# Kernel tuning notes

Measured on AMD Instinct MI355X. Metric: run time of the kernel, lower is better.

## Reference

```python
import jax, jax.numpy as jnp
import numpy as np

N_NODES = 50000
N_EDGES = 1_600_000
IN_FEAT = 64
HIDDEN = 64
OUT_FEAT = 10
NUM_LAYERS = 8
ALPHA = 0.1
THETA = 0.5
LN_EPS = 1e-5


def setup_inputs() -> dict:
    key = jax.random.key(0)
    ks = jax.random.split(key, 6)
    N, E, Fin, H, C = N_NODES, N_EDGES, IN_FEAT, HIDDEN, OUT_FEAT
    return {
        "x": jax.random.normal(ks[0], (N, Fin), jnp.float32),
        "W_lin": jax.random.normal(ks[1], (Fin, H), jnp.float32) / np.float32(np.sqrt(Fin)),
        "b_lin": jnp.zeros((H,), jnp.float32),
        "Ws": jax.random.normal(ks[2], (NUM_LAYERS, H, H), jnp.float32) / np.float32(np.sqrt(H)),
        "W1": jax.random.normal(ks[3], (2 * H, H), jnp.float32) / np.float32(np.sqrt(2 * H)),
        "b1": jnp.zeros((H,), jnp.float32),
        "ln_g": jnp.ones((H,), jnp.float32),
        "ln_b": jnp.zeros((H,), jnp.float32),
        "W2": jax.random.normal(ks[4], (H, C), jnp.float32) / np.float32(np.sqrt(H)),
        "b2": jnp.zeros((C,), jnp.float32),
        "edge_index": jax.random.randint(ks[5], (2, E), 0, N, jnp.int32),
    }


def _gcn_norm(edge_index, n):
    # PyG gcn_norm: add self-loops, symmetric D^-1/2 A D^-1/2 normalization.
    loop = jnp.arange(n, dtype=edge_index.dtype)
    row = jnp.concatenate([edge_index[0], loop])
    col = jnp.concatenate([edge_index[1], loop])
    w = jnp.ones(row.shape[0], jnp.float32)
    deg = jax.ops.segment_sum(w, col, num_segments=n)
    dinv = jnp.where(deg > 0, jax.lax.rsqrt(deg), 0.0)
    return row, col, dinv[row] * dinv[col]


def reference(x, W_lin, b_lin, Ws, W1, b1, ln_g, ln_b, W2, b2, edge_index):
    n = x.shape[0]
    row, col, vals = _gcn_norm(edge_index, n)
    h = jax.nn.relu(x @ W_lin + b_lin)  # [N, H]
    h0 = h
    for layer in range(NUM_LAYERS):
        beta = np.float32(np.log(THETA / (layer + 1) + 1.0))
        # SpMM: out[i] = sum over edges (i<-j) vals * h[j]
        agg = jax.ops.segment_sum(vals[:, None] * h[col], row, num_segments=n)
        mix = (1.0 - ALPHA) * agg + ALPHA * h0  # GCN2 initial-residual
        h = jax.nn.relu((1.0 - beta) * mix + beta * (mix @ Ws[layer]))  # identity mapping
    # mix_node_features 'cat': gather endpoint features per edge -> [E, 2H]
    line_x = jnp.concatenate([h[edge_index[0]], h[edge_index[1]]], axis=-1)
    # ClassifierMLP2: Linear -> LayerNorm -> ReLU -> Linear
    z = line_x @ W1 + b1
    mu = jnp.mean(z, axis=-1, keepdims=True)
    var = jnp.var(z, axis=-1, keepdims=True)
    z = (z - mu) * jax.lax.rsqrt(var + LN_EPS) * ln_g + ln_b
    z = jax.nn.relu(z)
    return z @ W2 + b2  # [E, out_features]
```

## Files before the change

### kernel.cpp

```cpp
#include <hip/hip_runtime.h>
#include <hip/hip_fp16.h>
#include <math.h>

#define N_NODES 50000
#define N_EDGES 1600000
#define EDGE_GRID 2048
#define CAP 128

#define NB 64
#define BRANGE 782
#define BCAP 28672
#define BIN_BLOCKS 512
#define EPB (N_EDGES/BIN_BLOCKS)
#define CURPAD 32

using half8  = __attribute__((ext_vector_type(8))) _Float16;
using half4  = __attribute__((ext_vector_type(4))) _Float16;
using float4v = __attribute__((ext_vector_type(4))) float;

__device__ __forceinline__ float rl(float v, int srclane){
  return __int_as_float(__builtin_amdgcn_readlane(__float_as_int(v), srclane));
}

__global__ __launch_bounds__(256) void k_bin(const int* __restrict__ rowE, const int* __restrict__ colE,
                                             unsigned* __restrict__ rstream, unsigned short* __restrict__ cstream,
                                             int* __restrict__ rcur, int* __restrict__ ccur){
  __shared__ int hr[NB], hc[NB], br[NB], bc[NB];
  int t = threadIdx.x;
  if(t < NB){ hr[t] = 0; hc[t] = 0; }
  __syncthreads();
  int e0 = blockIdx.x * EPB;
  for(int e = e0 + t; e < e0 + EPB; e += 256){
    int r = __builtin_nontemporal_load(rowE + e);
    int c = __builtin_nontemporal_load(colE + e);
    atomicAdd(&hr[r/BRANGE], 1);
    atomicAdd(&hc[c/BRANGE], 1);
  }
  __syncthreads();
  if(t < NB){
    br[t] = atomicAdd(&rcur[t*CURPAD], hr[t]); hr[t] = 0;
    bc[t] = atomicAdd(&ccur[t*CURPAD], hc[t]); hc[t] = 0;
  }
  __syncthreads();
  for(int e = e0 + t; e < e0 + EPB; e += 256){
    int r = rowE[e];
    int c = colE[e];
    int rb = r/BRANGE, cb = c/BRANGE;
    int rp = br[rb] + atomicAdd(&hr[rb], 1);
    int cp = bc[cb] + atomicAdd(&hc[cb], 1);
    if(rp < BCAP) rstream[(size_t)rb*BCAP + rp] = ((unsigned)r << 16) | (unsigned)c;
    if(cp < BCAP) cstream[(size_t)cb*BCAP + cp] = (unsigned short)c;
  }
}

__global__ __launch_bounds__(256) void k_build(const unsigned* __restrict__ rstream,
                                               const unsigned short* __restrict__ cstream,
                                               const int* __restrict__ rcur, const int* __restrict__ ccur,
                                               int* __restrict__ row_fill, int* __restrict__ degcnt,
                                               unsigned short* __restrict__ csr_col){
  __shared__ int lf[BRANGE];
  int b = blockIdx.x & (NB-1);
  int role = blockIdx.x >> 6;
  int base = b*BRANGE;
  int range = min(BRANGE, N_NODES - base);
  int t = threadIdx.x;
  for(int i=t;i<range;i+=256) lf[i] = 0;
  __syncthreads();
  if(role == 0){
    int cnt = min(rcur[b*CURPAD], BCAP);
    const unsigned* sp = rstream + (size_t)b*BCAP;
    for(int i=t;i<cnt;i+=256){
      unsigned rc = sp[i];
      int r = (int)(rc >> 16), c = (int)(rc & 0xffffu);
      int pos = atomicAdd(&lf[r-base], 1);
      if(pos < CAP) csr_col[(size_t)r*CAP + pos] = (unsigned short)c;
    }
    __syncthreads();
    for(int i=t;i<range;i+=256) row_fill[base+i] = lf[i];
  } else {
    int cnt = min(ccur[b*CURPAD], BCAP);
    const unsigned short* sp = cstream + (size_t)b*BCAP;
    for(int i=t;i<cnt;i+=256){
      int c = (int)sp[i];
      atomicAdd(&lf[c-base], 1);
    }
    __syncthreads();
    for(int i=t;i<range;i+=256) degcnt[base+i] = lf[i];
  }
}

__global__ void k_dinv(int* __restrict__ degcnt_rdeg, float* __restrict__ dinv,
                       __half* __restrict__ gA, __half* __restrict__ gB){
  int i = blockIdx.x*256 + threadIdx.x;
  if(i < N_NODES){
    float dp1 = (float)(degcnt_rdeg[i] + 1);
    dinv[i] = rsqrtf(dp1);
    ((float*)degcnt_rdeg)[i] = sqrtf(dp1);
  }
  if(i < 64){
    gA[(size_t)N_NODES*64 + i] = __float2half(0.f);
    gB[(size_t)N_NODES*64 + i] = __float2half(0.f);
  }
}


__global__ __launch_bounds__(256) void k_lin0(const float* __restrict__ x, const float* __restrict__ W,
                                              const float* __restrict__ b, const float* __restrict__ dinv,
                                              __half* __restrict__ h0, __half* __restrict__ g0){
  __shared__ float Wl[4096];
  int t = threadIdx.x;
  for(int i=t;i<4096;i+=256) Wl[i] = W[i];
  __syncthreads();
  int wave = t>>6, lane = t&63;
  int row0 = blockIdx.x*16 + wave*4;
  float4 xq = ((const float4*)(x + (size_t)row0*64))[lane];
  float a0=0,a1=0,a2=0,a3=0;
  #pragma unroll
  for(int k=0;k<64;k++){
    float w = Wl[k*64+lane];
    float comp = ((k&3)==0)?xq.x:((k&3)==1)?xq.y:((k&3)==2)?xq.z:xq.w;
    a0 += rl(comp,      (k>>2)) * w;
    a1 += rl(comp, 16 + (k>>2)) * w;
    a2 += rl(comp, 32 + (k>>2)) * w;
    a3 += rl(comp, 48 + (k>>2)) * w;
  }
  float bb = b[lane];
  float h[4] = {fmaxf(a0+bb,0.f), fmaxf(a1+bb,0.f), fmaxf(a2+bb,0.f), fmaxf(a3+bb,0.f)};
  #pragma unroll
  for(int r=0;r<4;r++){
    float dv = dinv[row0+r];
    h0[(size_t)(row0+r)*64+lane] = __float2half(h[r]);
    g0[(size_t)(row0+r)*64+lane] = __float2half(dv*h[r]);
  }
}

__global__ __launch_bounds__(256) void k_ab(const __half* __restrict__ g, const float* __restrict__ rdeg,
                                            const float* __restrict__ W1,
                                            __half* __restrict__ A, __half* __restrict__ B){
  __shared__ float Wa[4096];
  __shared__ float Wb[4096];
  int t = threadIdx.x;
  for(int i=t;i<4096;i+=256){ Wa[i] = W1[i]; Wb[i] = W1[4096+i]; }
  __syncthreads();
  int wave = t>>6, lane = t&63;
  int row0 = blockIdx.x*16 + wave*4;
  int myrow = row0 + (lane>>4);
  float rd = rdeg[myrow];
  const __half2* hp = (const __half2*)(g + (size_t)row0*64);
  __half2 p01 = hp[2*lane], p23 = hp[2*lane+1];
  float2 f01 = __half22float2(p01), f23 = __half22float2(p23);
  float4 xq = make_float4(f01.x*rd, f01.y*rd, f23.x*rd, f23.y*rd);
  float a0=0,a1=0,a2=0,a3=0,b0=0,b1=0,b2=0,b3=0;
  #pragma unroll
  for(int k=0;k<64;k++){
    float wa = Wa[k*64+lane], wb = Wb[k*64+lane];
    float comp = ((k&3)==0)?xq.x:((k&3)==1)?xq.y:((k&3)==2)?xq.z:xq.w;
    float s0 = rl(comp,      (k>>2));
    float s1 = rl(comp, 16 + (k>>2));
    float s2 = rl(comp, 32 + (k>>2));
    float s3 = rl(comp, 48 + (k>>2));
    a0 += s0*wa; a1 += s1*wa; a2 += s2*wa; a3 += s3*wa;
    b0 += s0*wb; b1 += s1*wb; b2 += s2*wb; b3 += s3*wb;
  }
  A[(size_t)(row0+0)*64+lane]=__float2half(a0); A[(size_t)(row0+1)*64+lane]=__float2half(a1);
  A[(size_t)(row0+2)*64+lane]=__float2half(a2); A[(size_t)(row0+3)*64+lane]=__float2half(a3);
  B[(size_t)(row0+0)*64+lane]=__float2half(b0); B[(size_t)(row0+1)*64+lane]=__float2half(b1);
  B[(size_t)(row0+2)*64+lane]=__float2half(b2); B[(size_t)(row0+3)*64+lane]=__float2half(b3);
}

__global__ __launch_bounds__(256) void k_layer(const __half* __restrict__ g_in, const __half* __restrict__ h0,
                          const int* __restrict__ row_fill, const unsigned short* __restrict__ csr_col,
                          const float* __restrict__ dinv,
                          const float* __restrict__ Wsl, float beta, __half* __restrict__ g_out){
  __shared__ __align__(16) _Float16 tile[16*72];
  int t = threadIdx.x, wave = t>>6, lane = t&63;
  int quad = lane>>4, l15 = lane&15;
  int grp = lane>>3, l8 = lane&7;

  half8 bfrag0, bfrag1;
  int n = 16*wave + l15;
  #pragma unroll
  for(int j=0;j<8;j++){
    int k0 = quad*8 + j;
    int k1 = 32 + quad*8 + j;
    float v0 = beta*Wsl[k0*64+n] + ((k0==n)?(1.f-beta):0.f);
    float v1 = beta*Wsl[k1*64+n] + ((k1==n)?(1.f-beta):0.f);
    bfrag0[j] = (_Float16)v0;
    bfrag1[j] = (_Float16)v1;
  }

  int i0 = blockIdx.x*16;
  int iw = i0 + 4*wave;

  int deg[4], cv[4];
  half8 selfv[4], h0v[4];
  float dv[4];
  #pragma unroll
  for(int r=0;r<4;r++) deg[r] = min(row_fill[iw+r], CAP);
  #pragma unroll
  for(int r=0;r<4;r++){
    const unsigned short* colp = csr_col + (size_t)(iw+r)*CAP;
    cv[r] = (lane < deg[r]) ? (int)__builtin_nontemporal_load(colp + lane) : 0;
  }
  #pragma unroll
  for(int r=0;r<4;r++){
    dv[r]    = dinv[iw+r];
    selfv[r] = *(const half8*)(g_in + (size_t)(iw+r)*64 + 8*l8);
    h0v[r]   = *(const half8*)(h0   + (size_t)(iw+r)*64 + 8*l8);
  }

  for(int r=0;r<4;r++){
    const unsigned short* colp = csr_col + (size_t)(iw+r)*CAP;
    float acc[8] = {0,0,0,0,0,0,0,0};
    int base = 0;
    int cur  = cv[r];
    for(;;){
      int rem = deg[r] - base; if(rem > 64) rem = 64;
      int nit = (rem + 7) >> 3;
      int it = 0;
      for(; it+2<=nit; it+=2){
        int iA = 8*it + grp, iB = iA + 8;
        int cA = __shfl(cur, iA, 64); cA = (iA < rem) ? cA : N_NODES;
        int cB = __shfl(cur, iB, 64); cB = (iB < rem) ? cB : N_NODES;
        half8 vA = *(const half8*)(g_in + (size_t)cA*64 + 8*l8);
        half8 vB = *(const half8*)(g_in + (size_t)cB*64 + 8*l8);
        #pragma unroll
        for(int k=0;k<8;k++) acc[k] += (float)vA[k] + (float)vB[k];
      }
      if(it < nit){
        int iA = 8*it + grp;
        int cA = __shfl(cur, iA, 64); cA = (iA < rem) ? cA : N_NODES;
        half8 vA = *(const half8*)(g_in + (size_t)cA*64 + 8*l8);
        #pragma unroll
        for(int k=0;k<8;k++) acc[k] += (float)vA[k];
      }
      base += 64;
      if(base >= deg[r]) break;
      cur = (base + lane < deg[r]) ? (int)__builtin_nontemporal_load(colp + base + lane) : 0;
    }
    #pragma unroll
    for(int k=0;k<8;k++){
      acc[k] += __shfl_xor(acc[k], 8, 64);
      acc[k] += __shfl_xor(acc[k], 16, 64);
      acc[k] += __shfl_xor(acc[k], 32, 64);
    }
    if(grp == 0){
      half8 mixv;
      #pragma unroll
      for(int k=0;k<8;k++){
        float m = 0.9f*dv[r]*(acc[k] + (float)selfv[r][k]) + 0.1f*(float)h0v[r][k];
        mixv[k] = (_Float16)m;
      }
      *(half8*)&tile[(4*wave+r)*72 + 8*l8] = mixv;
    }
  }
  __syncthreads();

  float4v acc4 = {0.f,0.f,0.f,0.f};
  half8 afrag0 = *(const half8*)&tile[l15*72 + quad*8];
  half8 afrag1 = *(const half8*)&tile[l15*72 + quad*8 + 32];
  acc4 = __builtin_amdgcn_mfma_f32_16x16x32_f16(afrag0, bfrag0, acc4, 0,0,0);
  acc4 = __builtin_amdgcn_mfma_f32_16x16x32_f16(afrag1, bfrag1, acc4, 0,0,0);
  #pragma unroll
  for(int r=0;r<4;r++){
    int row = quad*4 + r;
    float dvo = dinv[i0+row];
    g_out[(size_t)(i0+row)*64 + n] = __float2half(dvo*fmaxf(acc4[r], 0.f));
  }
}

__global__ __launch_bounds__(256) void k_edge(const __half* __restrict__ A, const __half* __restrict__ B,
                         const int* __restrict__ srcE, const int* __restrict__ dstE,
                         const float* __restrict__ b1v, const float* __restrict__ lng,
                         const float* __restrict__ lnb, const float* __restrict__ W2,
                         const float* __restrict__ b2v, float* __restrict__ out){
  int t = threadIdx.x, wave = t>>6, lane = t&63;
  int l15 = lane&15, quad = lane>>4;

  half8 bf0, bf1;
  #pragma unroll
  for(int j=0;j<8;j++){
    float w0 = (l15<10) ? W2[(quad*8+j)*10 + l15]    : 0.f;
    float w1 = (l15<10) ? W2[(32+quad*8+j)*10 + l15] : 0.f;
    bf0[j] = (_Float16)w0;
    bf1[j] = (_Float16)w1;
  }
  float b1r0[8], b1r1[8], gr0[8], gr1[8], br0[8], br1[8];
  #pragma unroll
  for(int j=0;j<8;j++){
    b1r0[j] = b1v[quad*8+j];    b1r1[j] = b1v[32+quad*8+j];
    gr0[j]  = lng[quad*8+j];    gr1[j]  = lng[32+quad*8+j];
    br0[j]  = lnb[quad*8+j];    br1[j]  = lnb[32+quad*8+j];
  }
  float bias = (l15<10) ? b2v[l15] : 0.f;

  for(int eb = blockIdx.x*64 + wave*16; eb < N_EDGES; eb += EDGE_GRID*64){
    int e = eb + l15;
    int s = __builtin_nontemporal_load(srcE + e);
    int d = __builtin_nontemporal_load(dstE + e);
    half8 a0 = *(const half8*)(A + (size_t)s*64 + quad*8);
    half8 a1 = *(const half8*)(A + (size_t)s*64 + 32 + quad*8);
    half8 g0 = *(const half8*)(B + (size_t)d*64 + quad*8);
    half8 g1 = *(const half8*)(B + (size_t)d*64 + 32 + quad*8);
    float z0[8], z1[8];
    float s1 = 0.f, s2 = 0.f;
    #pragma unroll
    for(int j=0;j<8;j++){
      float za = (float)a0[j] + (float)g0[j] + b1r0[j];
      float zb = (float)a1[j] + (float)g1[j] + b1r1[j];
      z0[j]=za; z1[j]=zb;
      s1 += za + zb;
      s2 += za*za + zb*zb;
    }
    s1 += __shfl_xor(s1,16,64); s1 += __shfl_xor(s1,32,64);
    s2 += __shfl_xor(s2,16,64); s2 += __shfl_xor(s2,32,64);
    float mu  = s1*(1.f/64.f);
    float var = s2*(1.f/64.f) - mu*mu;
    float rs  = rsqrtf(var + 1e-5f);
    half8 af0, af1;
    #pragma unroll
    for(int j=0;j<8;j++){
      af0[j] = (_Float16)fmaxf((z0[j]-mu)*rs*gr0[j] + br0[j], 0.f);
      af1[j] = (_Float16)fmaxf((z1[j]-mu)*rs*gr1[j] + br1[j], 0.f);
    }
    float4v acc = {0.f,0.f,0.f,0.f};
    acc = __builtin_amdgcn_mfma_f32_16x16x32_f16(af0, bf0, acc, 0,0,0);
    acc = __builtin_amdgcn_mfma_f32_16x16x32_f16(af1, bf1, acc, 0,0,0);
    if(l15 < 10){
      #pragma unroll
      for(int r=0;r<4;r++){
        __builtin_nontemporal_store(acc[r] + bias, &out[(size_t)(eb + quad*4 + r)*10 + l15]);
      }
    }
  }
}


extern "C" void kernel_launch(void* const* d_in, const int* in_sizes, int n_in,
                              void* d_out, int out_size, void* d_ws, size_t ws_size,
                              hipStream_t stream){
  const float* x     = (const float*)d_in[0];
  const float* W_lin = (const float*)d_in[1];
  const float* b_lin = (const float*)d_in[2];
  const float* Ws    = (const float*)d_in[3];
  const float* W1    = (const float*)d_in[4];
  const float* b1    = (const float*)d_in[5];
  const float* ln_g  = (const float*)d_in[6];
  const float* ln_b  = (const float*)d_in[7];
  const float* W2    = (const float*)d_in[8];
  const float* b2    = (const float*)d_in[9];
  const int*   eidx  = (const int*)d_in[10];
  const int*   rowE  = eidx;
  const int*   colE  = eidx + N_EDGES;
  float* out = (float*)d_out;

  char* ws = (char*)d_ws;
  size_t o = 0;
  auto alloc = [&](size_t bytes)->char*{ char* p = ws + o; o = (o + bytes + 255) & ~(size_t)255; return p; };
  int*   row_fill= (int*)  alloc((size_t)N_NODES*4);
  int*   degcnt  = (int*)  alloc((size_t)N_NODES*4);
  float* dinv    = (float*)alloc((size_t)N_NODES*4);
  unsigned short* csr_col = (unsigned short*)alloc((size_t)N_NODES*CAP*2);
  unsigned* rstream = (unsigned*)alloc((size_t)NB*BCAP*4);
  unsigned short* cstream = (unsigned short*)alloc((size_t)NB*BCAP*2);
  int*   rcur    = (int*)  alloc((size_t)NB*CURPAD*4);
  int*   ccur    = (int*)  alloc((size_t)NB*CURPAD*4);
  __half* h0     = (__half*)alloc((size_t)(N_NODES+1)*64*2);
  __half* gA     = (__half*)alloc((size_t)(N_NODES+1)*64*2);
  __half* gB     = (__half*)alloc((size_t)(N_NODES+1)*64*2);
  float* rdeg    = (float*)degcnt;

  hipMemsetAsync(rcur, 0, (size_t)NB*CURPAD*4, stream);
  hipMemsetAsync(ccur, 0, (size_t)NB*CURPAD*4, stream);

  k_bin  <<<BIN_BLOCKS, 256, 0, stream>>>(rowE, colE, rstream, cstream, rcur, ccur);
  k_build<<<2*NB, 256, 0, stream>>>(rstream, cstream, rcur, ccur, row_fill, degcnt, csr_col);
  k_dinv <<<(N_NODES+255)/256, 256, 0, stream>>>(degcnt, dinv, gA, gB);

  k_lin0<<<N_NODES/16, 256, 0, stream>>>(x, W_lin, b_lin, dinv, h0, gA);

  const __half* gin = gA;
  __half* bufs[2] = {gB, gA};
  for(int L=0; L<8; L++){
    float beta = logf(0.5f/(float)(L+1) + 1.0f);
    __half* gout = bufs[L&1];
    k_layer<<<(N_NODES+15)/16, 256, 0, stream>>>(gin, h0, row_fill, csr_col, dinv,
                                                 Ws + (size_t)L*4096, beta, gout);
    gin = gout;
  }
  __half* Abuf = gB;
  __half* Bbuf = h0;
  k_ab<<<N_NODES/16, 256, 0, stream>>>(gA, rdeg, W1, Abuf, Bbuf);
  k_edge<<<EDGE_GRID, 256, 0, stream>>>(Abuf, Bbuf, rowE, colE, b1, ln_g, ln_b, W2, b2, out);
}
```

Baseline: 550.6 us.

## Gather two CSR rows at once with 16-lane half4 groups in layer SpMM

New measurement: 530.6 us. 3.6% less time.

```diff
diff --git a/kernel.cpp b/kernel.cpp
--- a/kernel.cpp
+++ b/kernel.cpp
@@ -175,7 +175,6 @@
   __shared__ __align__(16) _Float16 tile[16*72];
   int t = threadIdx.x, wave = t>>6, lane = t&63;
   int quad = lane>>4, l15 = lane&15;
-  int grp = lane>>3, l8 = lane&7;
 
   half8 bfrag0, bfrag1;
   int n = 16*wave + l15;
@@ -183,17 +182,15 @@
   for(int j=0;j<8;j++){
     int k0 = quad*8 + j;
     int k1 = 32 + quad*8 + j;
-    float v0 = beta*Wsl[k0*64+n] + ((k0==n)?(1.f-beta):0.f);
-    float v1 = beta*Wsl[k1*64+n] + ((k1==n)?(1.f-beta):0.f);
-    bfrag0[j] = (_Float16)v0;
-    bfrag1[j] = (_Float16)v1;
+    bfrag0[j] = (_Float16)(beta*Wsl[k0*64+n] + ((k0==n)?(1.f-beta):0.f));
+    bfrag1[j] = (_Float16)(beta*Wsl[k1*64+n] + ((k1==n)?(1.f-beta):0.f));
   }
 
   int i0 = blockIdx.x*16;
   int iw = i0 + 4*wave;
 
   int deg[4], cv[4];
-  half8 selfv[4], h0v[4];
+  half4 selfv[4], h0v[4];
   float dv[4];
   #pragma unroll
   for(int r=0;r<4;r++) deg[r] = min(row_fill[iw+r], CAP);
@@ -205,53 +202,76 @@
   #pragma unroll
   for(int r=0;r<4;r++){
     dv[r]    = dinv[iw+r];
-    selfv[r] = *(const half8*)(g_in + (size_t)(iw+r)*64 + 8*l8);
-    h0v[r]   = *(const half8*)(h0   + (size_t)(iw+r)*64 + 8*l8);
-  }
-
-  for(int r=0;r<4;r++){
-    const unsigned short* colp = csr_col + (size_t)(iw+r)*CAP;
-    float acc[8] = {0,0,0,0,0,0,0,0};
-    int base = 0;
-    int cur  = cv[r];
-    for(;;){
-      int rem = deg[r] - base; if(rem > 64) rem = 64;
-      int nit = (rem + 7) >> 3;
-      int it = 0;
-      for(; it+2<=nit; it+=2){
-        int iA = 8*it + grp, iB = iA + 8;
-        int cA = __shfl(cur, iA, 64); cA = (iA < rem) ? cA : N_NODES;
-        int cB = __shfl(cur, iB, 64); cB = (iB < rem) ? cB : N_NODES;
-        half8 vA = *(const half8*)(g_in + (size_t)cA*64 + 8*l8);
-        half8 vB = *(const half8*)(g_in + (size_t)cB*64 + 8*l8);
-        #pragma unroll
-        for(int k=0;k<8;k++) acc[k] += (float)vA[k] + (float)vB[k];
+    selfv[r] = *(const half4*)(g_in + (size_t)(iw+r)*64 + 4*l15);
+    h0v[r]   = *(const half4*)(h0   + (size_t)(iw+r)*64 + 4*l15);
+  }
+
+  #pragma unroll
+  for(int p=0;p<2;p++){
+    const int rA = 2*p, rB = 2*p+1;
+    float4v aA = {0.f,0.f,0.f,0.f}, aB = {0.f,0.f,0.f,0.f};
+    int dA = min(deg[rA], 64), dB = min(deg[rB], 64);
+    int nit = (max(dA, dB) + 3) >> 2;
+    for(int it=0; it<nit; it+=4){
+      int j0 = 4*it + quad, j1 = j0+4, j2 = j0+8, j3 = j0+12;
+      int a0=__shfl(cv[rA], j0, 64); a0 = (j0<dA) ? a0 : N_NODES;
+      int a1=__shfl(cv[rA], j1, 64); a1 = (j1<dA) ? a1 : N_NODES;
+      int a2=__shfl(cv[rA], j2, 64); a2 = (j2<dA) ? a2 : N_NODES;
+      int a3=__shfl(cv[rA], j3, 64); a3 = (j3<dA) ? a3 : N_NODES;
+      int b0=__shfl(cv[rB], j0, 64); b0 = (j0<dB) ? b0 : N_NODES;
+      int b1=__shfl(cv[rB], j1, 64); b1 = (j1<dB) ? b1 : N_NODES;
+      int b2=__shfl(cv[rB], j2, 64); b2 = (j2<dB) ? b2 : N_NODES;
+      int b3=__shfl(cv[rB], j3, 64); b3 = (j3<dB) ? b3 : N_NODES;
+      half4 vA0 = *(const half4*)(g_in + (size_t)a0*64 + 4*l15);
+      half4 vA1 = *(const half4*)(g_in + (size_t)a1*64 + 4*l15);
+      half4 vA2 = *(const half4*)(g_in + (size_t)a2*64 + 4*l15);
+      half4 vA3 = *(const half4*)(g_in + (size_t)a3*64 + 4*l15);
+      half4 vB0 = *(const half4*)(g_in + (size_t)b0*64 + 4*l15);
+      half4 vB1 = *(const half4*)(g_in + (size_t)b1*64 + 4*l15);
+      half4 vB2 = *(const half4*)(g_in + (size_t)b2*64 + 4*l15);
+      half4 vB3 = *(const half4*)(g_in + (size_t)b3*64 + 4*l15);
+      #pragma unroll
+      for(int k=0;k<4;k++){
+        aA[k] += ((float)vA0[k]+(float)vA1[k]) + ((float)vA2[k]+(float)vA3[k]);
+        aB[k] += ((float)vB0[k]+(float)vB1[k]) + ((float)vB2[k]+(float)vB3[k]);
       }
-      if(it < nit){
-        int iA = 8*it + grp;
-        int cA = __shfl(cur, iA, 64); cA = (iA < rem) ? cA : N_NODES;
-        half8 vA = *(const half8*)(g_in + (size_t)cA*64 + 8*l8);
-        #pragma unroll
-        for(int k=0;k<8;k++) acc[k] += (float)vA[k];
+    }
+    #pragma unroll
+    for(int rr=0; rr<2; rr++){
+      const int r = 2*p + rr;
+      int dg = deg[r];
+      if(dg > 64){
+        const unsigned short* colp = csr_col + (size_t)(iw+r)*CAP;
+        int cur = (64 + lane < dg) ? (int)colp[64 + lane] : 0;
+        int rem = dg - 64;
+        int nit2 = (rem + 3) >> 2;
+        for(int it2=0; it2<nit2; it2++){
+          int j = 4*it2 + quad;
+          int c = __shfl(cur, j, 64); c = (j<rem) ? c : N_NODES;
+          half4 v = *(const half4*)(g_in + (size_t)c*64 + 4*l15);
+          #pragma unroll
+          for(int k=0;k<4;k++){
+            if(rr==0) aA[k] += (float)v[k]; else aB[k] += (float)v[k];
+          }
+        }
       }
-      base += 64;
-      if(base >= deg[r]) break;
-      cur = (base + lane < deg[r]) ? (int)__builtin_nontemporal_load(colp + base + lane) : 0;
     }
     #pragma unroll
-    for(int k=0;k<8;k++){
-      acc[k] += __shfl_xor(acc[k], 8, 64);
-      acc[k] += __shfl_xor(acc[k], 16, 64);
-      acc[k] += __shfl_xor(acc[k], 32, 64);
-    }
-    if(grp == 0){
-      half8 mixv;
+    for(int k=0;k<4;k++){
+      aA[k] += __shfl_xor(aA[k], 16, 64);
+      aA[k] += __shfl_xor(aA[k], 32, 64);
+      aB[k] += __shfl_xor(aB[k], 16, 64);
+      aB[k] += __shfl_xor(aB[k], 32, 64);
+    }
+    if(quad == 0){
+      half4 mA, mB;
       #pragma unroll
-      for(int k=0;k<8;k++){
-        float m = 0.9f*dv[r]*(acc[k] + (float)selfv[r][k]) + 0.1f*(float)h0v[r][k];
-        mixv[k] = (_Float16)m;
+      for(int k=0;k<4;k++){
+        mA[k] = (_Float16)(0.9f*dv[rA]*(aA[k] + (float)selfv[rA][k]) + 0.1f*(float)h0v[rA][k]);
+        mB[k] = (_Float16)(0.9f*dv[rB]*(aB[k] + (float)selfv[rB][k]) + 0.1f*(float)h0v[rB][k]);
       }
-      *(half8*)&tile[(4*wave+r)*72 + 8*l8] = mixv;
+      *(half4*)&tile[(4*wave+rA)*72 + 4*l15] = mA;
+      *(half4*)&tile[(4*wave+rB)*72 + 4*l15] = mB;
     }
   }
   __syncthreads();
```

## Split node features into two 32-wide halves for cache-resident SpMM gathers

Applied to the files above, without the earlier changes.

After: 643.3 us. 16.8% more time.

```diff
diff --git a/kernel.cpp b/kernel.cpp
--- a/kernel.cpp
+++ b/kernel.cpp
@@ -90,23 +90,27 @@
 }
 
 __global__ void k_dinv(int* __restrict__ degcnt_rdeg, float* __restrict__ dinv,
-                       __half* __restrict__ gA, __half* __restrict__ gB){
+                       __half* __restrict__ gAlo, __half* __restrict__ gAhi,
+                       __half* __restrict__ gBlo, __half* __restrict__ gBhi){
   int i = blockIdx.x*256 + threadIdx.x;
   if(i < N_NODES){
     float dp1 = (float)(degcnt_rdeg[i] + 1);
     dinv[i] = rsqrtf(dp1);
     ((float*)degcnt_rdeg)[i] = sqrtf(dp1);
   }
-  if(i < 64){
-    gA[(size_t)N_NODES*64 + i] = __float2half(0.f);
-    gB[(size_t)N_NODES*64 + i] = __float2half(0.f);
+  if(i < 32){
+    gAlo[(size_t)N_NODES*32 + i] = __float2half(0.f);
+    gAhi[(size_t)N_NODES*32 + i] = __float2half(0.f);
+    gBlo[(size_t)N_NODES*32 + i] = __float2half(0.f);
+    gBhi[(size_t)N_NODES*32 + i] = __float2half(0.f);
   }
 }
 
 
 __global__ __launch_bounds__(256) void k_lin0(const float* __restrict__ x, const float* __restrict__ W,
                                               const float* __restrict__ b, const float* __restrict__ dinv,
-                                              __half* __restrict__ h0, __half* __restrict__ g0){
+                                              __half* __restrict__ h0,
+                                              __half* __restrict__ gLo, __half* __restrict__ gHi){
   __shared__ float Wl[4096];
   int t = threadIdx.x;
   for(int i=t;i<4096;i+=256) Wl[i] = W[i];
@@ -130,11 +134,14 @@
   for(int r=0;r<4;r++){
     float dv = dinv[row0+r];
     h0[(size_t)(row0+r)*64+lane] = __float2half(h[r]);
-    g0[(size_t)(row0+r)*64+lane] = __float2half(dv*h[r]);
-  }
-}
-
-__global__ __launch_bounds__(256) void k_ab(const __half* __restrict__ g, const float* __restrict__ rdeg,
+    float gv = dv*h[r];
+    if(lane < 32) gLo[(size_t)(row0+r)*32 + lane]      = __float2half(gv);
+    else          gHi[(size_t)(row0+r)*32 + lane - 32] = __float2half(gv);
+  }
+}
+
+__global__ __launch_bounds__(256) void k_ab(const __half* __restrict__ gLo, const __half* __restrict__ gHi,
+                                            const float* __restrict__ rdeg,
                                             const float* __restrict__ W1,
                                             __half* __restrict__ A, __half* __restrict__ B){
   __shared__ float Wa[4096];
@@ -144,10 +151,12 @@
   __syncthreads();
   int wave = t>>6, lane = t&63;
   int row0 = blockIdx.x*16 + wave*4;
+  int l15 = lane&15;
   int myrow = row0 + (lane>>4);
   float rd = rdeg[myrow];
-  const __half2* hp = (const __half2*)(g + (size_t)row0*64);
-  __half2 p01 = hp[2*lane], p23 = hp[2*lane+1];
+  const __half* gp = (l15<8) ? (gLo + (size_t)myrow*32 + 4*l15)
+                             : (gHi + (size_t)myrow*32 + 4*(l15-8));
+  __half2 p01 = ((const __half2*)gp)[0], p23 = ((const __half2*)gp)[1];
   float2 f01 = __half22float2(p01), f23 = __half22float2(p23);
   float4 xq = make_float4(f01.x*rd, f01.y*rd, f23.x*rd, f23.y*rd);
   float a0=0,a1=0,a2=0,a3=0,b0=0,b1=0,b2=0,b3=0;
@@ -168,33 +177,14 @@
   B[(size_t)(row0+2)*64+lane]=__float2half(b2); B[(size_t)(row0+3)*64+lane]=__float2half(b3);
 }
 
-__global__ __launch_bounds__(256) void k_layer(const __half* __restrict__ g_in, const __half* __restrict__ h0,
+__global__ __launch_bounds__(256) void k_gather(const __half* __restrict__ gT,
                           const int* __restrict__ row_fill, const unsigned short* __restrict__ csr_col,
-                          const float* __restrict__ dinv,
-                          const float* __restrict__ Wsl, float beta, __half* __restrict__ g_out){
-  __shared__ __align__(16) _Float16 tile[16*72];
+                          float* __restrict__ agg){
   int t = threadIdx.x, wave = t>>6, lane = t&63;
-  int quad = lane>>4, l15 = lane&15;
   int grp = lane>>3, l8 = lane&7;
-
-  half8 bfrag0, bfrag1;
-  int n = 16*wave + l15;
-  #pragma unroll
-  for(int j=0;j<8;j++){
-    int k0 = quad*8 + j;
-    int k1 = 32 + quad*8 + j;
-    float v0 = beta*Wsl[k0*64+n] + ((k0==n)?(1.f-beta):0.f);
-    float v1 = beta*Wsl[k1*64+n] + ((k1==n)?(1.f-beta):0.f);
-    bfrag0[j] = (_Float16)v0;
-    bfrag1[j] = (_Float16)v1;
-  }
-
-  int i0 = blockIdx.x*16;
-  int iw = i0 + 4*wave;
+  int iw = blockIdx.x*16 + 4*wave;
 
   int deg[4], cv[4];
-  half8 selfv[4], h0v[4];
-  float dv[4];
   #pragma unroll
   for(int r=0;r<4;r++) deg[r] = min(row_fill[iw+r], CAP);
   #pragma unroll
@@ -202,16 +192,11 @@
     const unsigned short* colp = csr_col + (size_t)(iw+r)*CAP;
     cv[r] = (lane < deg[r]) ? (int)__builtin_nontemporal_load(colp + lane) : 0;
   }
-  #pragma unroll
-  for(int r=0;r<4;r++){
-    dv[r]    = dinv[iw+r];
-    selfv[r] = *(const half8*)(g_in + (size_t)(iw+r)*64 + 8*l8);
-    h0v[r]   = *(const half8*)(h0   + (size_t)(iw+r)*64 + 8*l8);
-  }
 
   for(int r=0;r<4;r++){
     const unsigned short* colp = csr_col + (size_t)(iw+r)*CAP;
-    float acc[8] = {0,0,0,0,0,0,0,0};
+    half4 selfv = *(const half4*)(gT + (size_t)(iw+r)*32 + 4*l8);
+    float4v acc = {0.f,0.f,0.f,0.f};
     int base = 0;
     int cur  = cv[r];
     for(;;){
@@ -222,36 +207,119 @@
         int iA = 8*it + grp, iB = iA + 8;
         int cA = __shfl(cur, iA, 64); cA = (iA < rem) ? cA : N_NODES;
         int cB = __shfl(cur, iB, 64); cB = (iB < rem) ? cB : N_NODES;
-        half8 vA = *(const half8*)(g_in + (size_t)cA*64 + 8*l8);
-        half8 vB = *(const half8*)(g_in + (size_t)cB*64 + 8*l8);
+        half4 vA = *(const half4*)(gT + (size_t)cA*32 + 4*l8);
+        half4 vB = *(const half4*)(gT + (size_t)cB*32 + 4*l8);
         #pragma unroll
-        for(int k=0;k<8;k++) acc[k] += (float)vA[k] + (float)vB[k];
+        for(int k=0;k<4;k++) acc[k] += (float)vA[k] + (float)vB[k];
       }
       if(it < nit){
         int iA = 8*it + grp;
         int cA = __shfl(cur, iA, 64); cA = (iA < rem) ? cA : N_NODES;
-        half8 vA = *(const half8*)(g_in + (size_t)cA*64 + 8*l8);
+        half4 vA = *(const half4*)(gT + (size_t)cA*32 + 4*l8);
         #pragma unroll
-        for(int k=0;k<8;k++) acc[k] += (float)vA[k];
+        for(int k=0;k<4;k++) acc[k] += (float)vA[k];
       }
       base += 64;
       if(base >= deg[r]) break;
       cur = (base + lane < deg[r]) ? (int)__builtin_nontemporal_load(colp + base + lane) : 0;
     }
     #pragma unroll
-    for(int k=0;k<8;k++){
-      acc[k] += __shfl_xor(acc[k], 8, 64);
+    for(int k=0;k<4;k++){
+      acc[k] += __shfl_xor(acc[k],  8, 64);
       acc[k] += __shfl_xor(acc[k], 16, 64);
       acc[k] += __shfl_xor(acc[k], 32, 64);
     }
     if(grp == 0){
-      half8 mixv;
+      float4v o;
       #pragma unroll
-      for(int k=0;k<8;k++){
-        float m = 0.9f*dv[r]*(acc[k] + (float)selfv[r][k]) + 0.1f*(float)h0v[r][k];
-        mixv[k] = (_Float16)m;
-      }
-      *(half8*)&tile[(4*wave+r)*72 + 8*l8] = mixv;
+      for(int k=0;k<4;k++) o[k] = acc[k] + (float)selfv[k];
+      __builtin_nontemporal_store(o, (float4v*)(agg + (size_t)(iw+r)*32 + 4*l8));
+    }
+  }
+}
+
+__global__ __launch_bounds__(256) void k_gmix(const __half* __restrict__ gT,
+                          const float* __restrict__ agg, const __half* __restrict__ h0,
+                          const int* __restrict__ row_fill, const unsigned short* __restrict__ csr_col,
+                          const float* __restrict__ dinv,
+                          const float* __restrict__ Wsl, float beta,
+                          __half* __restrict__ goLo, __half* __restrict__ goHi){
+  __shared__ __align__(16) _Float16 tile[16*72];
+  int t = threadIdx.x, wave = t>>6, lane = t&63;
+  int quad = lane>>4, l15 = lane&15;
+  int grp = lane>>3, l8 = lane&7;
+
+  half8 bfrag0, bfrag1;
+  int n = 16*wave + l15;
+  #pragma unroll
+  for(int j=0;j<8;j++){
+    int k0 = quad*8 + j;
+    int k1 = 32 + quad*8 + j;
+    bfrag0[j] = (_Float16)(beta*Wsl[k0*64+n] + ((k0==n)?(1.f-beta):0.f));
+    bfrag1[j] = (_Float16)(beta*Wsl[k1*64+n] + ((k1==n)?(1.f-beta):0.f));
+  }
+
+  int i0 = blockIdx.x*16;
+  int iw = i0 + 4*wave;
+
+  int deg[4], cv[4];
+  #pragma unroll
+  for(int r=0;r<4;r++) deg[r] = min(row_fill[iw+r], CAP);
+  #pragma unroll
+  for(int r=0;r<4;r++){
+    const unsigned short* colp = csr_col + (size_t)(iw+r)*CAP;
+    cv[r] = (lane < deg[r]) ? (int)__builtin_nontemporal_load(colp + lane) : 0;
+  }
+
+  for(int r=0;r<4;r++){
+    const unsigned short* colp = csr_col + (size_t)(iw+r)*CAP;
+    half4 selfv = *(const half4*)(gT + (size_t)(iw+r)*32 + 4*l8);
+    half4 h0lo  = *(const half4*)(h0 + (size_t)(iw+r)*64 + 4*l8);
+    half4 h0hi  = *(const half4*)(h0 + (size_t)(iw+r)*64 + 32 + 4*l8);
+    float4v al  = *(const float4v*)(agg + (size_t)(iw+r)*32 + 4*l8);
+    float dv    = dinv[iw+r];
+    float4v acc = {0.f,0.f,0.f,0.f};
+    int base = 0;
+    int cur  = cv[r];
+    for(;;){
+      int rem = deg[r] - base; if(rem > 64) rem = 64;
+      int nit = (rem + 7) >> 3;
+      int it = 0;
+      for(; it+2<=nit; it+=2){
+        int iA = 8*it + grp, iB = iA + 8;
+        int cA = __shfl(cur, iA, 64); cA = (iA < rem) ? cA : N_NODES;
+        int cB = __shfl(cur, iB, 64); cB = (iB < rem) ? cB : N_NODES;
+        half4 vA = *(const half4*)(gT + (size_t)cA*32 + 4*l8);
+        half4 vB = *(const half4*)(gT + (size_t)cB*32 + 4*l8);
+        #pragma unroll
+        for(int k=0;k<4;k++) acc[k] += (float)vA[k] + (float)vB[k];
+      }
+      if(it < nit){
+        int iA = 8*it + grp;
+        int cA = __shfl(cur, iA, 64); cA = (iA < rem) ? cA : N_NODES;
+        half4 vA = *(const half4*)(gT + (size_t)cA*32 + 4*l8);
+        #pragma unroll
+        for(int k=0;k<4;k++) acc[k] += (float)vA[k];
+      }
+      base += 64;
+      if(base >= deg[r]) break;
+      cur = (base + lane < deg[r]) ? (int)__builtin_nontemporal_load(colp + base + lane) : 0;
+    }
+    #pragma unroll
+    for(int k=0;k<4;k++){
+      acc[k] += __shfl_xor(acc[k],  8, 64);
+      acc[k] += __shfl_xor(acc[k], 16, 64);
+      acc[k] += __shfl_xor(acc[k], 32, 64);
+    }
+    if(grp == 0){
+      half4 mLo, mHi;
+      #pragma unroll
+      for(int k=0;k<4;k++){
+        mLo[k] = (_Float16)(0.9f*dv*al[k]                      + 0.1f*(float)h0lo[k]);
+        mHi[k] = (_Float16)(0.9f*dv*(acc[k] + (float)selfv[k]) + 0.1f*(float)h0hi[k]);
+      }
+      *(half4*)&tile[(4*wave+r)*72 + 4*l8]      = mLo;
+      *(half4*)&tile[(4*wave+r)*72 + 32 + 4*l8] = mHi;
     }
   }
   __syncthreads();
@@ -261,11 +329,12 @@
   half8 afrag1 = *(const half8*)&tile[l15*72 + quad*8 + 32];
   acc4 = __builtin_amdgcn_mfma_f32_16x16x32_f16(afrag0, bfrag0, acc4, 0,0,0);
   acc4 = __builtin_amdgcn_mfma_f32_16x16x32_f16(afrag1, bfrag1, acc4, 0,0,0);
+  __half* outp = (n < 32) ? (goLo + n) : (goHi + (n - 32));
   #pragma unroll
   for(int r=0;r<4;r++){
     int row = quad*4 + r;
     float dvo = dinv[i0+row];
-    g_out[(size_t)(i0+row)*64 + n] = __float2half(dvo*fmaxf(acc4[r], 0.f));
+    outp[(size_t)(i0+row)*32] = __float2half(dvo*fmaxf(acc4[r], 0.f));
   }
 }
 
@@ -366,8 +435,12 @@
   int*   rcur    = (int*)  alloc((size_t)NB*CURPAD*4);
   int*   ccur    = (int*)  alloc((size_t)NB*CURPAD*4);
   __half* h0     = (__half*)alloc((size_t)(N_NODES+1)*64*2);
-  __half* gA     = (__half*)alloc((size_t)(N_NODES+1)*64*2);
-  __half* gB     = (__half*)alloc((size_t)(N_NODES+1)*64*2);
+  __half* gAlo   = (__half*)alloc((size_t)(N_NODES+1)*32*2);
+  __half* gAhi   = (__half*)alloc((size_t)(N_NODES+1)*32*2);
+  __half* gBlo   = (__half*)alloc((size_t)(N_NODES+1)*32*2);
+  __half* gBhi   = (__half*)alloc((size_t)(N_NODES+1)*32*2);
+  float* agg     = (float*)alloc((size_t)N_NODES*32*4);
+  __half* Abuf   = (__half*)alloc((size_t)N_NODES*64*2);
   float* rdeg    = (float*)degcnt;
 
   hipMemsetAsync(rcur, 0, (size_t)NB*CURPAD*4, stream);
@@ -375,21 +448,22 @@
 
   k_bin  <<<BIN_BLOCKS, 256, 0, stream>>>(rowE, colE, rstream, cstream, rcur, ccur);
   k_build<<<2*NB, 256, 0, stream>>>(rstream, cstream, rcur, ccur, row_fill, degcnt, csr_col);
-  k_dinv <<<(N_NODES+255)/256, 256, 0, stream>>>(degcnt, dinv, gA, gB);
-
-  k_lin0<<<N_NODES/16, 256, 0, stream>>>(x, W_lin, b_lin, dinv, h0, gA);
-
-  const __half* gin = gA;
-  __half* bufs[2] = {gB, gA};
+  k_dinv <<<(N_NODES+255)/256, 256, 0, stream>>>(degcnt, dinv, gAlo, gAhi, gBlo, gBhi);
+
+  k_lin0<<<N_NODES/16, 256, 0, stream>>>(x, W_lin, b_lin, dinv, h0, gAlo, gAhi);
+
+  const __half* ginLo = gAlo; const __half* ginHi = gAhi;
+  __half* loBufs[2] = {gBlo, gAlo};
+  __half* hiBufs[2] = {gBhi, gAhi};
   for(int L=0; L<8; L++){
     float beta = logf(0.5f/(float)(L+1) + 1.0f);
-    __half* gout = bufs[L&1];
-    k_layer<<<(N_NODES+15)/16, 256, 0, stream>>>(gin, h0, row_fill, csr_col, dinv,
-                                                 Ws + (size_t)L*4096, beta, gout);
-    gin = gout;
-  }
-  __half* Abuf = gB;
+    k_gather<<<(N_NODES+15)/16, 256, 0, stream>>>(ginLo, row_fill, csr_col, agg);
+    k_gmix  <<<(N_NODES+15)/16, 256, 0, stream>>>(ginHi, agg, h0, row_fill, csr_col, dinv,
+                                                  Ws + (size_t)L*4096, beta,
+                                                  loBufs[L&1], hiBufs[L&1]);
+    ginLo = loBufs[L&1]; ginHi = hiBufs[L&1];
+  }
   __half* Bbuf = h0;
-  k_ab<<<N_NODES/16, 256, 0, stream>>>(gA, rdeg, W1, Abuf, Bbuf);
+  k_ab<<<N_NODES/16, 256, 0, stream>>>(gAlo, gAhi, rdeg, W1, Abuf, Bbuf);
   k_edge<<<EDGE_GRID, 256, 0, stream>>>(Abuf, Bbuf, rowE, colE, b1, ln_g, ln_b, W2, b2, out);
 }
```
